# Kernel optimization log

Hardware: AMD Instinct MI355X
Metric: run time of the kernel (lower is better)

Reference implementation:

```python
import jax, jax.numpy as jnp
import numpy as np

_LN_EPS = 1e-5

def _gelu(x):
    return jax.nn.gelu(x, approximate=False)

def _layernorm(x, g, b):
    mu = x.mean(-1, keepdims=True)
    var = ((x - mu) ** 2).mean(-1, keepdims=True)
    return (x - mu) * jax.lax.rsqrt(var + _LN_EPS) * g + b

def setup_inputs() -> dict:
    key = jax.random.key(0)
    ks = jax.random.split(key, 8)
    B, S, D = 4, 2048, 1024
    N_IN, N_PROC, D_R = 8192, 4096, 256
    s = 0.02
    return {
        "x": jax.random.normal(ks[0], (B, S, D), jnp.float32),
        "W1": jax.random.normal(ks[1], (2 * D_R, D), jnp.float32) * s,
        "b1": jnp.zeros((2 * D_R,), jnp.float32),
        "ln_g": jnp.ones((2 * D_R,), jnp.float32),
        "ln_b": jnp.zeros((2 * D_R,), jnp.float32),
        "W2": jax.random.normal(ks[2], (D_R, 2 * D_R), jnp.float32) * s,
        "b2": jnp.zeros((D_R,), jnp.float32),
        "neuron_keys": jax.random.normal(ks[3], (N_IN, D_R), jnp.float32) * s,
        "input_patterns": jax.random.normal(ks[4], (N_IN, D), jnp.float32) * s,
        "process_weights": jax.random.normal(ks[5], (N_PROC, N_IN), jnp.float32) * s,
        "process_outputs": jax.random.normal(ks[6], (N_PROC, D), jnp.float32) * s,
        "k_input": 4096,
        "k_process": 2048,
    }

def reference(x, W1, b1, ln_g, ln_b, W2, b2, neuron_keys, input_patterns,
              process_weights, process_outputs, k_input, k_process):
    d_routing = neuron_keys.shape[1]
    # --- Global router: sequence max-pool context -> query -> top-k input neurons
    gc = x.max(axis=1)                                   # [B, D]
    h = _layernorm(_gelu(gc @ W1.T + b1), ln_g, ln_b)    # [B, 2*d_r]
    query = h @ W2.T + b2                                # [B, d_r]
    logits = (query @ neuron_keys.T) / jnp.sqrt(jnp.asarray(d_routing, x.dtype))  # [B, N_in]
    _, input_idx = jax.lax.top_k(logits, k_input)        # [B, k_in]
    # --- Input neuron activations, gather selected ones
    input_acts = _gelu(jnp.einsum('bsd,nd->bsn', x, input_patterns))   # [B,S,N_in]
    sel_acts = jnp.take_along_axis(input_acts, input_idx[:, None, :], axis=2)  # [B,S,k_in]
    # --- Per-batch gather of process weight columns, process activations
    W_sel = jnp.take(process_weights, input_idx, axis=1)               # [N_proc,B,k_in]
    proc_acts = _gelu(jnp.einsum('bsk,pbk->bsp', sel_acts, W_sel))     # [B,S,N_proc]
    scores = proc_acts.mean(axis=1)                                    # [B,N_proc]
    _, proc_idx = jax.lax.top_k(scores, k_process)                     # [B,k_proc]
    sel_proc = jnp.take_along_axis(proc_acts, proc_idx[:, None, :], axis=2)  # [B,S,k_proc]
    out_w = process_outputs[proc_idx]                                  # [B,k_proc,D]
    return jnp.einsum('bsk,bkd->bsd', sel_proc, out_w)                 # [B,S,D]
```

## Files before the change

kernel.cpp:

```cpp
#include <hip/hip_runtime.h>
#include <cstdint>

#define B_    4
#define S_    2048
#define D_    1024
#define NIN   8192
#define NPROC 4096
#define DR    256
#define DR2   512
#define KIN   4096
#define KPROC 2048

typedef _Float16 v8h  __attribute__((ext_vector_type(8)));
typedef _Float16 v4h  __attribute__((ext_vector_type(4)));
typedef float    v4f  __attribute__((ext_vector_type(4)));
typedef float    v16f __attribute__((ext_vector_type(16)));

__device__ __forceinline__ float geluf(float v) {
    return 0.5f * v * (1.0f + erff(v * 0.70710678f));
}

__device__ __forceinline__ void cp16(void* lds, const void* g) {
    __builtin_amdgcn_global_load_lds(
        (const __attribute__((address_space(1))) unsigned int*)g,
        (__attribute__((address_space(3))) unsigned int*)lds, 16, 0, 0);
}

__global__ void k_conv_x16(const float* __restrict__ x, _Float16* __restrict__ x16, int n4) {
    int i = blockIdx.x * 256 + threadIdx.x;
    if (i < n4) {
        float4 v = ((const float4*)x)[i];
        v4h h = { (_Float16)v.x, (_Float16)v.y, (_Float16)v.z, (_Float16)v.w };
        ((v4h*)x16)[i] = h;
    }
}

__global__ void k_conv_split(const float* __restrict__ p, _Float16* __restrict__ ph,
                             _Float16* __restrict__ pl, int n) {
    int i = blockIdx.x * 256 + threadIdx.x;
    if (i < n) {
        float v = p[i];
        _Float16 h = (_Float16)v;
        ph[i] = h;
        pl[i] = (_Float16)(v - (float)h);
    }
}

__global__ void k_max1(const float* __restrict__ x, float* __restrict__ pmax) {
    int d = blockIdx.x * 256 + threadIdx.x;
    int chunk = blockIdx.y;
    int b = blockIdx.z;
    const float* base = x + ((size_t)b * S_ + chunk * 128) * D_ + d;
    float m = -3.4e38f;
    for (int s = 0; s < 128; s++) m = fmaxf(m, base[(size_t)s * D_]);
    pmax[((size_t)b * 16 + chunk) * D_ + d] = m;
}

__global__ void k_max2(const float* __restrict__ pmax, double* __restrict__ gc64) {
    int d = blockIdx.x * 256 + threadIdx.x;
    int b = blockIdx.y;
    float m = -3.4e38f;
    for (int c = 0; c < 16; c++) m = fmaxf(m, pmax[((size_t)b * 16 + c) * D_ + d]);
    gc64[(size_t)b * D_ + d] = (double)m;
}

__global__ __launch_bounds__(256) void k_router1(
    const double* __restrict__ gc64, const float* __restrict__ W1, const float* __restrict__ b1,
    double* __restrict__ hpre)
{
    int wave = threadIdx.x >> 6, lane = threadIdx.x & 63;
    int j = blockIdx.x * 4 + wave;
    int b = blockIdx.y;
    const double* g = gc64 + (size_t)b * D_;
    const float* w = W1 + (size_t)j * D_;
    double acc = 0.0;
    for (int d = lane; d < D_; d += 64) acc += g[d] * (double)w[d];
#pragma unroll
    for (int o = 32; o > 0; o >>= 1) acc += __shfl_xor(acc, o, 64);
    if (lane == 0) {
        double z = acc + (double)b1[j];
        hpre[(size_t)b * DR2 + j] = 0.5 * z * (1.0 + erf(z * 0.7071067811865475244));
    }
}

__global__ __launch_bounds__(512) void k_router2(
    const double* __restrict__ hpre, const float* __restrict__ lng, const float* __restrict__ lnb,
    const float* __restrict__ W2, const float* __restrict__ b2, double* __restrict__ qs)
{
    __shared__ double sh[DR2];
    __shared__ double red[DR2];
    int b = blockIdx.x, j = threadIdx.x;
    double ge = hpre[(size_t)b * DR2 + j];
    sh[j] = ge; red[j] = ge;
    __syncthreads();
    for (int s = 256; s > 0; s >>= 1) { if (j < s) red[j] += red[j + s]; __syncthreads(); }
    double mu = red[0] / 512.0;
    __syncthreads();
    double dv = ge - mu;
    red[j] = dv * dv;
    __syncthreads();
    for (int s = 256; s > 0; s >>= 1) { if (j < s) red[j] += red[j + s]; __syncthreads(); }
    double rs = 1.0 / sqrt(red[0] / 512.0 + 1e-5);
    __syncthreads();
    sh[j] = dv * rs * (double)lng[j] + (double)lnb[j];
    __syncthreads();
    if (j < DR) {
        double q = (double)b2[j];
        const float* w2r = W2 + (size_t)j * DR2;
        for (int t = 0; t < DR2; t++) q += sh[t] * (double)w2r[t];
        qs[(size_t)b * DR + j] = q;
    }
}

__global__ __launch_bounds__(256) void k_router3(
    const double* __restrict__ qs, const float* __restrict__ keys, double* __restrict__ logits)
{
    int wave = threadIdx.x >> 6, lane = threadIdx.x & 63;
    int n = blockIdx.x * 4 + wave;
    int b = blockIdx.y;
    const double* q = qs + (size_t)b * DR;
    const float* kr = keys + (size_t)n * DR;
    double acc = 0.0;
#pragma unroll
    for (int t = 0; t < 4; t++) {
        int d = lane + t * 64;
        acc += q[d] * (double)kr[d];
    }
#pragma unroll
    for (int o = 32; o > 0; o >>= 1) acc += __shfl_xor(acc, o, 64);
    if (lane == 0) logits[(size_t)b * NIN + n] = acc * 0.0625;
}

template<int N, int K>
__global__ __launch_bounds__(1024) void k_topk(const double* __restrict__ vals, int* __restrict__ outIdx) {
    __shared__ unsigned long long keys[N];
    int b = blockIdx.x, tid = threadIdx.x;
    for (int i = tid; i < N; i += 1024) {
        float v = (float)vals[(size_t)b * N + i];
        unsigned int u = __float_as_uint(v);
        u = (u & 0x80000000u) ? ~u : (u | 0x80000000u);
        keys[i] = ((unsigned long long)u << 32) | (unsigned int)(~i);
    }
    __syncthreads();
    for (int k = 2; k <= N; k <<= 1)
        for (int j = k >> 1; j > 0; j >>= 1) {
            for (int i = tid; i < N; i += 1024) {
                int l = i ^ j;
                if (l > i) {
                    unsigned long long a = keys[i], c = keys[l];
                    bool up = ((i & k) == 0);
                    if ((a < c) == up) { keys[i] = c; keys[l] = a; }
                }
            }
            __syncthreads();
        }
    for (int i = tid; i < K; i += 1024)
        outIdx[(size_t)b * K + i] = (int)(~(unsigned int)keys[i]);
}

__device__ __forceinline__ void dev_gatherW(const float* __restrict__ pw, const int* __restrict__ iidx,
                                            _Float16* __restrict__ Wh, _Float16* __restrict__ Wl,
                                            int p, int b, size_t bstride) {
    const float* row = pw + (size_t)p * NIN;
    const int* ix = iidx + (size_t)b * KIN;
    _Float16* wh = Wh + bstride + (size_t)p * KIN;
    _Float16* wl = Wl + bstride + (size_t)p * KIN;
    for (int j = threadIdx.x; j < KIN; j += 256) {
        float w = row[ix[j]];
        _Float16 h = (_Float16)w;
        wh[j] = h;
        wl[j] = (_Float16)(w - (float)h);
    }
}

__global__ void k_gatherSP(const _Float16* __restrict__ acts16, const int* __restrict__ pidx,
                           _Float16* __restrict__ sp) {
    int s = blockIdx.x, b = blockIdx.y;
    const _Float16* arow = acts16 + ((size_t)b * S_ + s) * NPROC;
    _Float16* orow = sp + ((size_t)b * S_ + s) * KPROC;
    const int* pi = pidx + (size_t)b * KPROC;
    for (int k = threadIdx.x; k < KPROC; k += 256) orow[k] = arow[pi[k]];
}

__global__ void k_gatherWoT(const _Float16* __restrict__ pout16, const int* __restrict__ pidx,
                            _Float16* __restrict__ woT) {
    __shared__ _Float16 t[64][65];
    int k0 = blockIdx.x * 64, d0 = blockIdx.y * 64, b = blockIdx.z;
    const int* pi = pidx + (size_t)b * KPROC;
    for (int i = threadIdx.x; i < 4096; i += 256) {
        int kk = i >> 6, dd = i & 63;
        t[kk][dd] = pout16[(size_t)pi[k0 + kk] * D_ + d0 + dd];
    }
    __syncthreads();
    for (int i = threadIdx.x; i < 4096; i += 256) {
        int dd = i >> 6, kk = i & 63;
        woT[((size_t)b * D_ + d0 + dd) * KPROC + k0 + kk] = t[kk][dd];
    }
}


__device__ __forceinline__ void dev_gemmD(
    const _Float16* __restrict__ x16, const _Float16* __restrict__ ph, const _Float16* __restrict__ pl,
    const int* __restrict__ iidx, _Float16* __restrict__ a16,
    _Float16* tA, _Float16* tBh, _Float16* tBl, int bx, int by, int b)
{
    const int m0 = bx * 128, n0 = by * 128;
    const int tid = threadIdx.x, lane = tid & 63;
    const int wave = tid >> 6, wrow = wave >> 1, wcol = wave & 1;
    const int srow = tid >> 2, spart = tid & 3;
    const int spe = spart ^ ((srow >> 1) & 3);

    const _Float16* as0 = x16 + ((size_t)b * S_ + m0 + srow) * D_ + spe * 8;
    const _Float16* as1 = as0 + (size_t)64 * D_;
    int r0 = iidx[(size_t)b * KIN + n0 + srow];
    int r1 = iidx[(size_t)b * KIN + n0 + srow + 64];
    const _Float16* bh0 = ph + (size_t)r0 * D_ + spe * 8;
    const _Float16* bh1 = ph + (size_t)r1 * D_ + spe * 8;
    const _Float16* bl0 = pl + (size_t)r0 * D_ + spe * 8;
    const _Float16* bl1 = pl + (size_t)r1 * D_ + spe * 8;

    v16f acc[2][2];
#pragma unroll
    for (int i = 0; i < 2; i++)
#pragma unroll
        for (int j = 0; j < 2; j++) acc[i][j] = (v16f)(0.0f);

    const int lrow = lane & 31, lhi = lane >> 5;
    const int swz = (lane >> 1) & 3;
    const int abase = (wrow * 64 + lrow) * 32;
    const int bbase = (wcol * 64 + lrow) * 32;

    cp16(&tA[tid * 8], as0);
    cp16(&tA[2048 + tid * 8], as1);
    cp16(&tBh[tid * 8], bh0);
    cp16(&tBh[2048 + tid * 8], bh1);
    cp16(&tBl[tid * 8], bl0);
    cp16(&tBl[2048 + tid * 8], bl1);
    asm volatile("s_waitcnt vmcnt(0)" ::: "memory");
    __syncthreads();

    for (int kt = 0; kt < D_; kt += 32) {
        const int cur = (kt >> 5) & 1;
        const int o = cur * 4096;
        if (kt + 32 < D_) {
            const int on = (cur ^ 1) * 4096;
            const int kn = kt + 32;
            cp16(&tA[on + tid * 8], as0 + kn);
            cp16(&tA[on + 2048 + tid * 8], as1 + kn);
            cp16(&tBh[on + tid * 8], bh0 + kn);
            cp16(&tBh[on + 2048 + tid * 8], bh1 + kn);
            cp16(&tBl[on + tid * 8], bl0 + kn);
            cp16(&tBl[on + 2048 + tid * 8], bl1 + kn);
        }
        v8h af[2][2], fh[2][2], fl[2][2];
#pragma unroll
        for (int kw = 0; kw < 2; kw++) {
            const int ch = ((kw * 2 + lhi) ^ swz) * 8;
#pragma unroll
            for (int mi = 0; mi < 2; mi++) af[mi][kw] = *(const v8h*)&tA[o + abase + mi * 1024 + ch];
#pragma unroll
            for (int nj = 0; nj < 2; nj++) {
                fh[nj][kw] = *(const v8h*)&tBh[o + bbase + nj * 1024 + ch];
                fl[nj][kw] = *(const v8h*)&tBl[o + bbase + nj * 1024 + ch];
            }
        }
#pragma unroll
        for (int kw = 0; kw < 2; kw++)
#pragma unroll
            for (int mi = 0; mi < 2; mi++)
#pragma unroll
                for (int nj = 0; nj < 2; nj++) {
                    acc[mi][nj] = __builtin_amdgcn_mfma_f32_32x32x16_f16(af[mi][kw], fh[nj][kw], acc[mi][nj], 0, 0, 0);
                    acc[mi][nj] = __builtin_amdgcn_mfma_f32_32x32x16_f16(af[mi][kw], fl[nj][kw], acc[mi][nj], 0, 0, 0);
                }
        asm volatile("s_waitcnt vmcnt(0)" ::: "memory");
        __syncthreads();
    }
#pragma unroll
    for (int mi = 0; mi < 2; mi++)
#pragma unroll
        for (int nj = 0; nj < 2; nj++)
#pragma unroll
            for (int r = 0; r < 16; r++) {
                int row = (r & 3) + 8 * (r >> 2) + 4 * lhi;
                float gv = geluf(acc[mi][nj][r]);
                a16[((size_t)b * S_ + m0 + wrow * 64 + mi * 32 + row) * (size_t)KIN
                    + n0 + wcol * 64 + nj * 32 + lrow] = (_Float16)gv;
            }
}

__global__ __launch_bounds__(256, 3) void k_gemmD(
    const _Float16* __restrict__ x16, const _Float16* __restrict__ ph, const _Float16* __restrict__ pl,
    const int* __restrict__ iidx, _Float16* __restrict__ a16)
{
    __shared__ _Float16 tA[8192], tBh[8192], tBl[8192];
    dev_gemmD(x16, ph, pl, iidx, a16, tA, tBh, tBl, blockIdx.x, blockIdx.y, blockIdx.z);
}

__global__ __launch_bounds__(256, 3) void k_fusedDW(
    const _Float16* __restrict__ x16, const _Float16* __restrict__ ph, const _Float16* __restrict__ pl,
    const int* __restrict__ iidx, _Float16* __restrict__ a16,
    const float* __restrict__ pw, _Float16* __restrict__ Wh, _Float16* __restrict__ Wl, size_t wstride)
{
    __shared__ _Float16 tA[8192], tBh[8192], tBl[8192];
    if (blockIdx.z >= 4) {
        int idx = (blockIdx.z - 4) * 512 + blockIdx.y * 16 + blockIdx.x;
        int p = idx >> 2, b = idx & 3;
        dev_gatherW(pw, iidx, Wh, Wl, p, b, (size_t)b * wstride);
        return;
    }
    dev_gemmD(x16, ph, pl, iidx, a16, tA, tBh, tBl, blockIdx.x, blockIdx.y, blockIdx.z);
}

__global__ void k_gatherW(const float* __restrict__ pw, const int* __restrict__ iidx,
                          _Float16* __restrict__ Wh, _Float16* __restrict__ Wl,
                          int b_base, size_t wstride) {
    dev_gatherW(pw, iidx, Wh, Wl, blockIdx.x, b_base + blockIdx.y, (size_t)blockIdx.y * wstride);
}

__global__ __launch_bounds__(256, 3) void k_gemmE(
    const _Float16* __restrict__ a16, const _Float16* __restrict__ Wh, const _Float16* __restrict__ Wl,
    _Float16* __restrict__ acts16, double* __restrict__ scores, int b_base, size_t wstride)
{
    const int b = b_base + blockIdx.z;
    const int m0 = blockIdx.x * 128, n0 = blockIdx.y * 128;
    __shared__ _Float16 tA[8192], tBh[8192], tBl[8192];
    const int tid = threadIdx.x, lane = tid & 63;
    const int wave = tid >> 6, wrow = wave >> 1, wcol = wave & 1;
    const int srow = tid >> 2, spart = tid & 3;
    const int spe = spart ^ ((srow >> 1) & 3);

    const _Float16* as0 = a16 + ((size_t)b * S_ + m0 + srow) * (size_t)KIN + spe * 8;
    const _Float16* as1 = as0 + (size_t)64 * KIN;
    const _Float16* whB = Wh + (size_t)blockIdx.z * wstride;
    const _Float16* wlB = Wl + (size_t)blockIdx.z * wstride;
    const _Float16* bh0 = whB + (size_t)(n0 + srow) * KIN + spe * 8;
    const _Float16* bh1 = bh0 + (size_t)64 * KIN;
    const _Float16* bl0 = wlB + (size_t)(n0 + srow) * KIN + spe * 8;
    const _Float16* bl1 = bl0 + (size_t)64 * KIN;

    v16f acc[2][2];
#pragma unroll
    for (int i = 0; i < 2; i++)
#pragma unroll
        for (int j = 0; j < 2; j++) acc[i][j] = (v16f)(0.0f);

    const int lrow = lane & 31, lhi = lane >> 5;
    const int swz = (lane >> 1) & 3;
    const int abase = (wrow * 64 + lrow) * 32;
    const int bbase = (wcol * 64 + lrow) * 32;

    cp16(&tA[tid * 8], as0);
    cp16(&tA[2048 + tid * 8], as1);
    cp16(&tBh[tid * 8], bh0);
    cp16(&tBh[2048 + tid * 8], bh1);
    cp16(&tBl[tid * 8], bl0);
    cp16(&tBl[2048 + tid * 8], bl1);
    asm volatile("s_waitcnt vmcnt(0)" ::: "memory");
    __syncthreads();

    for (int kt = 0; kt < KIN; kt += 32) {
        const int cur = (kt >> 5) & 1;
        const int o = cur * 4096;
        if (kt + 32 < KIN) {
            const int on = (cur ^ 1) * 4096;
            const int kn = kt + 32;
            cp16(&tA[on + tid * 8], as0 + kn);
            cp16(&tA[on + 2048 + tid * 8], as1 + kn);
            cp16(&tBh[on + tid * 8], bh0 + kn);
            cp16(&tBh[on + 2048 + tid * 8], bh1 + kn);
            cp16(&tBl[on + tid * 8], bl0 + kn);
            cp16(&tBl[on + 2048 + tid * 8], bl1 + kn);
        }
        v8h af[2][2], fh[2][2], fl[2][2];
#pragma unroll
        for (int kw = 0; kw < 2; kw++) {
            const int ch = ((kw * 2 + lhi) ^ swz) * 8;
#pragma unroll
            for (int mi = 0; mi < 2; mi++) af[mi][kw] = *(const v8h*)&tA[o + abase + mi * 1024 + ch];
#pragma unroll
            for (int nj = 0; nj < 2; nj++) {
                fh[nj][kw] = *(const v8h*)&tBh[o + bbase + nj * 1024 + ch];
                fl[nj][kw] = *(const v8h*)&tBl[o + bbase + nj * 1024 + ch];
            }
        }
#pragma unroll
        for (int kw = 0; kw < 2; kw++)
#pragma unroll
            for (int mi = 0; mi < 2; mi++)
#pragma unroll
                for (int nj = 0; nj < 2; nj++) {
                    acc[mi][nj] = __builtin_amdgcn_mfma_f32_32x32x16_f16(af[mi][kw], fh[nj][kw], acc[mi][nj], 0, 0, 0);
                    acc[mi][nj] = __builtin_amdgcn_mfma_f32_32x32x16_f16(af[mi][kw], fl[nj][kw], acc[mi][nj], 0, 0, 0);
                }
        asm volatile("s_waitcnt vmcnt(0)" ::: "memory");
        __syncthreads();
    }
    float psum[2] = {0.f, 0.f};
#pragma unroll
    for (int mi = 0; mi < 2; mi++)
#pragma unroll
        for (int nj = 0; nj < 2; nj++)
#pragma unroll
            for (int r = 0; r < 16; r++) {
                int row = (r & 3) + 8 * (r >> 2) + 4 * lhi;
                float gv = geluf(acc[mi][nj][r]);
                acts16[((size_t)b * S_ + m0 + wrow * 64 + mi * 32 + row) * (size_t)NPROC
                       + n0 + wcol * 64 + nj * 32 + lrow] = (_Float16)gv;
                psum[nj] += gv;
            }
#pragma unroll
    for (int nj = 0; nj < 2; nj++) {
        float s = psum[nj];
        s += __shfl_xor(s, 32, 64);
        if (lhi == 0)
            atomicAdd(&scores[(size_t)b * NPROC + n0 + wcol * 64 + nj * 32 + lrow], (double)s);
    }
}

__global__ __launch_bounds__(256, 3) void k_gemmF(
    const _Float16* __restrict__ sp, const _Float16* __restrict__ woT, float* __restrict__ out)
{
    const int b = blockIdx.z;
    const int m0 = blockIdx.x * 128, n0 = blockIdx.y * 128;
    __shared__ _Float16 tA[8192], tB[8192];
    const int tid = threadIdx.x, lane = tid & 63;
    const int wave = tid >> 6, wrow = wave >> 1, wcol = wave & 1;
    const int srow = tid >> 2, spart = tid & 3;
    const int spe = spart ^ ((srow >> 1) & 3);

    const _Float16* as0 = sp + ((size_t)b * S_ + m0 + srow) * (size_t)KPROC + spe * 8;
    const _Float16* as1 = as0 + (size_t)64 * KPROC;
    const _Float16* bs0 = woT + ((size_t)b * D_ + n0 + srow) * (size_t)KPROC + spe * 8;
    const _Float16* bs1 = bs0 + (size_t)64 * KPROC;

    v16f acc[2][2];
#pragma unroll
    for (int i = 0; i < 2; i++)
#pragma unroll
        for (int j = 0; j < 2; j++) acc[i][j] = (v16f)(0.0f);

    const int lrow = lane & 31, lhi = lane >> 5;
    const int swz = (lane >> 1) & 3;
    const int abase = (wrow * 64 + lrow) * 32;
    const int bbase = (wcol * 64 + lrow) * 32;

    cp16(&tA[tid * 8], as0);
    cp16(&tA[2048 + tid * 8], as1);
    cp16(&tB[tid * 8], bs0);
    cp16(&tB[2048 + tid * 8], bs1);
    asm volatile("s_waitcnt vmcnt(0)" ::: "memory");
    __syncthreads();

    for (int kt = 0; kt < KPROC; kt += 32) {
        const int cur = (kt >> 5) & 1;
        const int o = cur * 4096;
        if (kt + 32 < KPROC) {
            const int on = (cur ^ 1) * 4096;
            const int kn = kt + 32;
            cp16(&tA[on + tid * 8], as0 + kn);
            cp16(&tA[on + 2048 + tid * 8], as1 + kn);
            cp16(&tB[on + tid * 8], bs0 + kn);
            cp16(&tB[on + 2048 + tid * 8], bs1 + kn);
        }
        v8h af[2][2], bf[2][2];
#pragma unroll
        for (int kw = 0; kw < 2; kw++) {
            const int ch = ((kw * 2 + lhi) ^ swz) * 8;
#pragma unroll
            for (int mi = 0; mi < 2; mi++) af[mi][kw] = *(const v8h*)&tA[o + abase + mi * 1024 + ch];
#pragma unroll
            for (int nj = 0; nj < 2; nj++) bf[nj][kw] = *(const v8h*)&tB[o + bbase + nj * 1024 + ch];
        }
#pragma unroll
        for (int kw = 0; kw < 2; kw++)
#pragma unroll
            for (int mi = 0; mi < 2; mi++)
#pragma unroll
                for (int nj = 0; nj < 2; nj++)
                    acc[mi][nj] = __builtin_amdgcn_mfma_f32_32x32x16_f16(af[mi][kw], bf[nj][kw], acc[mi][nj], 0, 0, 0);
        asm volatile("s_waitcnt vmcnt(0)" ::: "memory");
        __syncthreads();
    }
#pragma unroll
    for (int mi = 0; mi < 2; mi++)
#pragma unroll
        for (int nj = 0; nj < 2; nj++)
#pragma unroll
            for (int r = 0; r < 16; r++) {
                int row = (r & 3) + 8 * (r >> 2) + 4 * lhi;
                out[((size_t)b * S_ + m0 + wrow * 64 + mi * 32 + row) * (size_t)D_
                    + n0 + wcol * 64 + nj * 32 + lrow] = acc[mi][nj][r];
            }
}

extern "C" void kernel_launch(void* const* d_in, const int* in_sizes, int n_in,
                              void* d_out, int out_size, void* d_ws, size_t ws_size,
                              hipStream_t stream) {
    const float* x    = (const float*)d_in[0];
    const float* W1   = (const float*)d_in[1];
    const float* b1   = (const float*)d_in[2];
    const float* lng  = (const float*)d_in[3];
    const float* lnb  = (const float*)d_in[4];
    const float* W2   = (const float*)d_in[5];
    const float* b2   = (const float*)d_in[6];
    const float* keys = (const float*)d_in[7];
    const float* patt = (const float*)d_in[8];
    const float* pw   = (const float*)d_in[9];
    const float* pout = (const float*)d_in[10];
    (void)in_sizes; (void)n_in; (void)out_size;

    char* w = (char*)d_ws;
    size_t off = 0;
    auto alloc = [&](size_t bytes) -> void* {
        void* p = w + off;
        off += (bytes + 255) & ~(size_t)255;
        return p;
    };
    double* gc64   = (double*)alloc((size_t)B_ * D_ * 8);
    float*  pmax   = (float*) alloc((size_t)B_ * 16 * D_ * 4);
    double* logits = (double*)alloc((size_t)B_ * NIN * 8);
    double* scores = (double*)alloc((size_t)B_ * NPROC * 8);
    double* hpre   = (double*)alloc((size_t)B_ * DR2 * 8);
    double* qs     = (double*)alloc((size_t)B_ * DR * 8);
    int*    iidx   = (int*)   alloc((size_t)B_ * KIN * 4);
    int*    pidx   = (int*)   alloc((size_t)B_ * KPROC * 4);
    _Float16* a16    = (_Float16*)alloc((size_t)B_ * S_ * KIN * 2);
    _Float16* acts16 = (_Float16*)alloc((size_t)B_ * S_ * NPROC * 2);
    _Float16* pout16 = (_Float16*)alloc((size_t)NPROC * D_ * 2);
    char* u1 = (char*)alloc((size_t)67108864);
    _Float16* x16 = (_Float16*)u1;
    _Float16* ph  = (_Float16*)(u1 + 16777216);
    _Float16* pl  = (_Float16*)(u1 + 33554432);
    _Float16* WhT = (_Float16*)u1;
    _Float16* WlT = (_Float16*)(u1 + 33554432);
    _Float16* sp  = (_Float16*)u1;
    _Float16* woT = (_Float16*)(u1 + 33554432);

    const size_t WSTRIDE = (size_t)NPROC * KIN;
    size_t off_before_fat = off;
    _Float16* WhA = (_Float16*)alloc((size_t)B_ * WSTRIDE * 2);
    _Float16* WlA = (_Float16*)alloc((size_t)B_ * WSTRIDE * 2);
    bool fat = (off <= ws_size);
    if (!fat) off = off_before_fat;

    hipMemsetAsync(scores, 0, (size_t)B_ * NPROC * 8, stream);

    k_conv_x16 <<<dim3((B_ * S_ * D_ / 4 + 255) / 256), 256, 0, stream>>>(x, x16, B_ * S_ * D_ / 4);
    k_conv_split<<<dim3((NIN * D_ + 255) / 256), 256, 0, stream>>>(patt, ph, pl, NIN * D_);
    k_conv_x16 <<<dim3((NPROC * D_ / 4 + 255) / 256), 256, 0, stream>>>(pout, pout16, NPROC * D_ / 4);

    k_max1<<<dim3(4, 16, 4), 256, 0, stream>>>(x, pmax);
    k_max2<<<dim3(4, 4), 256, 0, stream>>>(pmax, gc64);
    k_router1<<<dim3(128, 4), 256, 0, stream>>>(gc64, W1, b1, hpre);
    k_router2<<<dim3(4), 512, 0, stream>>>(hpre, lng, lnb, W2, b2, qs);
    k_router3<<<dim3(2048, 4), 256, 0, stream>>>(qs, keys, logits);
    k_topk<NIN, KIN><<<dim3(4), 1024, 0, stream>>>(logits, iidx);

    if (fat) {
        k_fusedDW<<<dim3(16, 32, 36), 256, 0, stream>>>(x16, ph, pl, iidx, a16, pw, WhA, WlA, WSTRIDE);
        k_gemmE<<<dim3(16, 32, 4), 256, 0, stream>>>(a16, WhA, WlA, acts16, scores, 0, WSTRIDE);
    } else {
        k_gemmD<<<dim3(16, 32, 4), 256, 0, stream>>>(x16, ph, pl, iidx, a16);
        for (int b = 0; b < 4; b++) {
            k_gatherW<<<dim3(NPROC, 1), 256, 0, stream>>>(pw, iidx, WhT, WlT, b, 0);
            k_gemmE<<<dim3(16, 32, 1), 256, 0, stream>>>(a16, WhT, WlT, acts16, scores, b, 0);
        }
    }

    k_topk<NPROC, KPROC><<<dim3(4), 1024, 0, stream>>>(scores, pidx);
    k_gatherSP<<<dim3(S_, 4), 256, 0, stream>>>(acts16, pidx, sp);
    k_gatherWoT<<<dim3(KPROC / 64, D_ / 64, 4), 256, 0, stream>>>(pout16, pidx, woT);
    k_gemmF<<<dim3(16, 8, 4), 256, 0, stream>>>(sp, woT, (float*)d_out);
}
```

Measured before the change: 1.574 ms.

## Restructure GEMM mainloops to prefetch two tiles ahead with partial vmcnt waits

In all three MFMA GEMM kernels the double-buffered loop is restructured so that two K-tiles are in flight. Each iteration waits only for the oldest tile with a partial vmcnt, reads fragments into registers, then barriers and issues the next global-to-LDS load into the just-freed buffer before running the MFMAs. The goal is to overlap global load latency with compute instead of draining all loads at the end of every iteration. In exchange it adds a second barrier per iteration and depends on exact vmcnt counts matching the number of cp16 loads issued, which would break silently if the load count changes.

```diff
diff --git a/kernel.cpp b/kernel.cpp
--- a/kernel.cpp
+++ b/kernel.cpp
@@ -230,28 +230,26 @@
     const int abase = (wrow * 64 + lrow) * 32;
     const int bbase = (wcol * 64 + lrow) * 32;
 
+    const int nt = D_ / 32;
     cp16(&tA[tid * 8], as0);
     cp16(&tA[2048 + tid * 8], as1);
     cp16(&tBh[tid * 8], bh0);
     cp16(&tBh[2048 + tid * 8], bh1);
     cp16(&tBl[tid * 8], bl0);
     cp16(&tBl[2048 + tid * 8], bl1);
-    asm volatile("s_waitcnt vmcnt(0)" ::: "memory");
-    __syncthreads();
-
-    for (int kt = 0; kt < D_; kt += 32) {
-        const int cur = (kt >> 5) & 1;
-        const int o = cur * 4096;
-        if (kt + 32 < D_) {
-            const int on = (cur ^ 1) * 4096;
-            const int kn = kt + 32;
-            cp16(&tA[on + tid * 8], as0 + kn);
-            cp16(&tA[on + 2048 + tid * 8], as1 + kn);
-            cp16(&tBh[on + tid * 8], bh0 + kn);
-            cp16(&tBh[on + 2048 + tid * 8], bh1 + kn);
-            cp16(&tBl[on + tid * 8], bl0 + kn);
-            cp16(&tBl[on + 2048 + tid * 8], bl1 + kn);
-        }
+    cp16(&tA[4096 + tid * 8], as0 + 32);
+    cp16(&tA[4096 + 2048 + tid * 8], as1 + 32);
+    cp16(&tBh[4096 + tid * 8], bh0 + 32);
+    cp16(&tBh[4096 + 2048 + tid * 8], bh1 + 32);
+    cp16(&tBl[4096 + tid * 8], bl0 + 32);
+    cp16(&tBl[4096 + 2048 + tid * 8], bl1 + 32);
+
+    for (int t = 0; t < nt; t++) {
+        const int o = (t & 1) * 4096;
+        if (t + 1 < nt) { asm volatile("s_waitcnt vmcnt(6)" ::: "memory"); }
+        else            { asm volatile("s_waitcnt vmcnt(0)" ::: "memory"); }
+        __builtin_amdgcn_s_barrier();
+        __builtin_amdgcn_sched_barrier(0);
         v8h af[2][2], fh[2][2], fl[2][2];
 #pragma unroll
         for (int kw = 0; kw < 2; kw++) {
@@ -264,6 +262,20 @@
                 fl[nj][kw] = *(const v8h*)&tBl[o + bbase + nj * 1024 + ch];
             }
         }
+        asm volatile("s_waitcnt lgkmcnt(0)" ::: "memory");
+        __builtin_amdgcn_sched_barrier(0);
+        __builtin_amdgcn_s_barrier();
+        __builtin_amdgcn_sched_barrier(0);
+        if (t + 2 < nt) {
+            const int kn = (t + 2) * 32;
+            cp16(&tA[o + tid * 8], as0 + kn);
+            cp16(&tA[o + 2048 + tid * 8], as1 + kn);
+            cp16(&tBh[o + tid * 8], bh0 + kn);
+            cp16(&tBh[o + 2048 + tid * 8], bh1 + kn);
+            cp16(&tBl[o + tid * 8], bl0 + kn);
+            cp16(&tBl[o + 2048 + tid * 8], bl1 + kn);
+        }
+        __builtin_amdgcn_sched_barrier(0);
 #pragma unroll
         for (int kw = 0; kw < 2; kw++)
 #pragma unroll
@@ -273,8 +285,6 @@
                     acc[mi][nj] = __builtin_amdgcn_mfma_f32_32x32x16_f16(af[mi][kw], fh[nj][kw], acc[mi][nj], 0, 0, 0);
                     acc[mi][nj] = __builtin_amdgcn_mfma_f32_32x32x16_f16(af[mi][kw], fl[nj][kw], acc[mi][nj], 0, 0, 0);
                 }
-        asm volatile("s_waitcnt vmcnt(0)" ::: "memory");
-        __syncthreads();
     }
 #pragma unroll
     for (int mi = 0; mi < 2; mi++)
@@ -350,28 +360,26 @@
     const int abase = (wrow * 64 + lrow) * 32;
     const int bbase = (wcol * 64 + lrow) * 32;
 
+    const int nt = KIN / 32;
     cp16(&tA[tid * 8], as0);
     cp16(&tA[2048 + tid * 8], as1);
     cp16(&tBh[tid * 8], bh0);
     cp16(&tBh[2048 + tid * 8], bh1);
     cp16(&tBl[tid * 8], bl0);
     cp16(&tBl[2048 + tid * 8], bl1);
-    asm volatile("s_waitcnt vmcnt(0)" ::: "memory");
-    __syncthreads();
-
-    for (int kt = 0; kt < KIN; kt += 32) {
-        const int cur = (kt >> 5) & 1;
-        const int o = cur * 4096;
-        if (kt + 32 < KIN) {
-            const int on = (cur ^ 1) * 4096;
-            const int kn = kt + 32;
-            cp16(&tA[on + tid * 8], as0 + kn);
-            cp16(&tA[on + 2048 + tid * 8], as1 + kn);
-            cp16(&tBh[on + tid * 8], bh0 + kn);
-            cp16(&tBh[on + 2048 + tid * 8], bh1 + kn);
-            cp16(&tBl[on + tid * 8], bl0 + kn);
-            cp16(&tBl[on + 2048 + tid * 8], bl1 + kn);
-        }
+    cp16(&tA[4096 + tid * 8], as0 + 32);
+    cp16(&tA[4096 + 2048 + tid * 8], as1 + 32);
+    cp16(&tBh[4096 + tid * 8], bh0 + 32);
+    cp16(&tBh[4096 + 2048 + tid * 8], bh1 + 32);
+    cp16(&tBl[4096 + tid * 8], bl0 + 32);
+    cp16(&tBl[4096 + 2048 + tid * 8], bl1 + 32);
+
+    for (int t = 0; t < nt; t++) {
+        const int o = (t & 1) * 4096;
+        if (t + 1 < nt) { asm volatile("s_waitcnt vmcnt(6)" ::: "memory"); }
+        else            { asm volatile("s_waitcnt vmcnt(0)" ::: "memory"); }
+        __builtin_amdgcn_s_barrier();
+        __builtin_amdgcn_sched_barrier(0);
         v8h af[2][2], fh[2][2], fl[2][2];
 #pragma unroll
         for (int kw = 0; kw < 2; kw++) {
@@ -384,6 +392,20 @@
                 fl[nj][kw] = *(const v8h*)&tBl[o + bbase + nj * 1024 + ch];
             }
         }
+        asm volatile("s_waitcnt lgkmcnt(0)" ::: "memory");
+        __builtin_amdgcn_sched_barrier(0);
+        __builtin_amdgcn_s_barrier();
+        __builtin_amdgcn_sched_barrier(0);
+        if (t + 2 < nt) {
+            const int kn = (t + 2) * 32;
+            cp16(&tA[o + tid * 8], as0 + kn);
+            cp16(&tA[o + 2048 + tid * 8], as1 + kn);
+            cp16(&tBh[o + tid * 8], bh0 + kn);
+            cp16(&tBh[o + 2048 + tid * 8], bh1 + kn);
+            cp16(&tBl[o + tid * 8], bl0 + kn);
+            cp16(&tBl[o + 2048 + tid * 8], bl1 + kn);
+        }
+        __builtin_amdgcn_sched_barrier(0);
 #pragma unroll
         for (int kw = 0; kw < 2; kw++)
 #pragma unroll
@@ -393,8 +415,6 @@
                     acc[mi][nj] = __builtin_amdgcn_mfma_f32_32x32x16_f16(af[mi][kw], fh[nj][kw], acc[mi][nj], 0, 0, 0);
                     acc[mi][nj] = __builtin_amdgcn_mfma_f32_32x32x16_f16(af[mi][kw], fl[nj][kw], acc[mi][nj], 0, 0, 0);
                 }
-        asm volatile("s_waitcnt vmcnt(0)" ::: "memory");
-        __syncthreads();
     }
     float psum[2] = {0.f, 0.f};
 #pragma unroll
@@ -445,24 +465,22 @@
     const int abase = (wrow * 64 + lrow) * 32;
     const int bbase = (wcol * 64 + lrow) * 32;
 
+    const int nt = KPROC / 32;
     cp16(&tA[tid * 8], as0);
     cp16(&tA[2048 + tid * 8], as1);
     cp16(&tB[tid * 8], bs0);
     cp16(&tB[2048 + tid * 8], bs1);
-    asm volatile("s_waitcnt vmcnt(0)" ::: "memory");
-    __syncthreads();
-
-    for (int kt = 0; kt < KPROC; kt += 32) {
-        const int cur = (kt >> 5) & 1;
-        const int o = cur * 4096;
-        if (kt + 32 < KPROC) {
-            const int on = (cur ^ 1) * 4096;
-            const int kn = kt + 32;
-            cp16(&tA[on + tid * 8], as0 + kn);
-            cp16(&tA[on + 2048 + tid * 8], as1 + kn);
-            cp16(&tB[on + tid * 8], bs0 + kn);
-            cp16(&tB[on + 2048 + tid * 8], bs1 + kn);
-        }
+    cp16(&tA[4096 + tid * 8], as0 + 32);
+    cp16(&tA[4096 + 2048 + tid * 8], as1 + 32);
+    cp16(&tB[4096 + tid * 8], bs0 + 32);
+    cp16(&tB[4096 + 2048 + tid * 8], bs1 + 32);
+
+    for (int t = 0; t < nt; t++) {
+        const int o = (t & 1) * 4096;
+        if (t + 1 < nt) { asm volatile("s_waitcnt vmcnt(4)" ::: "memory"); }
+        else            { asm volatile("s_waitcnt vmcnt(0)" ::: "memory"); }
+        __builtin_amdgcn_s_barrier();
+        __builtin_amdgcn_sched_barrier(0);
         v8h af[2][2], bf[2][2];
 #pragma unroll
         for (int kw = 0; kw < 2; kw++) {
@@ -472,6 +490,18 @@
 #pragma unroll
             for (int nj = 0; nj < 2; nj++) bf[nj][kw] = *(const v8h*)&tB[o + bbase + nj * 1024 + ch];
         }
+        asm volatile("s_waitcnt lgkmcnt(0)" ::: "memory");
+        __builtin_amdgcn_sched_barrier(0);
+        __builtin_amdgcn_s_barrier();
+        __builtin_amdgcn_sched_barrier(0);
+        if (t + 2 < nt) {
+            const int kn = (t + 2) * 32;
+            cp16(&tA[o + tid * 8], as0 + kn);
+            cp16(&tA[o + 2048 + tid * 8], as1 + kn);
+            cp16(&tB[o + tid * 8], bs0 + kn);
+            cp16(&tB[o + 2048 + tid * 8], bs1 + kn);
+        }
+        __builtin_amdgcn_sched_barrier(0);
 #pragma unroll
         for (int kw = 0; kw < 2; kw++)
 #pragma unroll
@@ -479,8 +509,6 @@
 #pragma unroll
                 for (int nj = 0; nj < 2; nj++)
                     acc[mi][nj] = __builtin_amdgcn_mfma_f32_32x32x16_f16(af[mi][kw], bf[nj][kw], acc[mi][nj], 0, 0, 0);
-        asm volatile("s_waitcnt vmcnt(0)" ::: "memory");
-        __syncthreads();
     }
 #pragma unroll
     for (int mi = 0; mi < 2; mi++)
```

Result: no change. 1.547 ms (-1.7%).
